# Kernel tuning notes

Hardware: AMD Instinct MI355X
Metric: run time of the kernel (lower is better)

## Reference

```python
import jax, jax.numpy as jnp
import numpy as np

N_NODES = 50000
N_EDGES = 800000
HID = 64
OUT = 64
REL = 5


def setup_inputs() -> dict:
    key = jax.random.key(0)
    ks = jax.random.split(key, 9)
    s_in = 1.0 / np.sqrt(HID)
    return {
        "contagion_risk": jax.random.normal(ks[0], (N_NODES, HID), jnp.float32),
        "edge_weight": jax.random.uniform(ks[1], (N_EDGES,), jnp.float32),
        # torch Linear weights stored transposed as [in, out] so y = x @ W + b
        "W_in_w": jax.random.uniform(ks[2], (HID, HID), jnp.float32, -s_in, s_in),
        "W_in_b": jax.random.uniform(ks[3], (HID,), jnp.float32, -s_in, s_in),
        "W_rel": jax.random.uniform(ks[4], (REL, HID, HID), jnp.float32, -s_in, s_in),
        "W_out_w": jax.random.uniform(ks[5], (HID, OUT), jnp.float32, -s_in, s_in),
        "W_out_b": jax.random.uniform(ks[6], (OUT,), jnp.float32, -s_in, s_in),
        "edge_index": jax.random.randint(ks[7], (2, N_EDGES), 0, N_NODES, jnp.int64 if jax.config.jax_enable_x64 else jnp.int32),
        "edge_type": jax.random.randint(ks[8], (N_EDGES,), 0, REL, jnp.int32),
        "num_nodes": N_NODES,
    }


def _dan_forward(contagion_risk, W_in_w, W_in_b, W_rel, W_out_w, W_out_b,
                 edge_index, edge_type, num_nodes):
    row, col = edge_index[0], edge_index[1]  # dst, src
    x = contagion_risk @ W_in_w + W_in_b                       # [N, H]
    x_j = x[col]                                               # [E, H] gather

    # gcn_norm (no self loops, unit edge weights): deg over col
    ones = jnp.ones(col.shape[0], x.dtype)
    deg = jax.ops.segment_sum(ones, col, num_segments=num_nodes)
    dis = jnp.where(deg > 0, jax.lax.rsqrt(jnp.maximum(deg, 1.0)), 0.0)
    norm_w = (dis[row] * dis[col])[:, None]                    # [E, 1]
    msg_gcn = jax.ops.segment_sum(x_j * norm_w, row, num_segments=num_nodes)

    # per-relation masked GEMM (grouped GEMM over REL relation types)
    res = jnp.zeros_like(x_j)
    for i in range(W_rel.shape[0]):
        mask = (edge_type == i)[:, None]
        res = res + jnp.where(mask, x_j @ W_rel[i], 0.0)

    # segment softmax over destination-node groups (per feature channel)
    seg_max = jax.ops.segment_max(res, row, num_segments=num_nodes)
    e = jnp.exp(res - seg_max[row])
    seg_sum = jax.ops.segment_sum(e, row, num_segments=num_nodes)
    weig = e / (seg_sum[row] + 1e-16)

    msg = jax.ops.segment_sum(res * weig, row, num_segments=num_nodes)
    out = (msg_gcn + 0.5 * jax.nn.relu(msg)) @ W_out_w + W_out_b
    return out


def reference(contagion_risk, edge_weight, W_in_w, W_in_b, W_rel, W_out_w, W_out_b,
              edge_index, edge_type, num_nodes):
    # edge_weight is accepted by the original forward but never used
    return _dan_forward(contagion_risk, W_in_w, W_in_b, W_rel, W_out_w, W_out_b,
                        edge_index, edge_type, num_nodes)
```

## Files before the change

### kernel.cpp

```cpp
#include <hip/hip_runtime.h>
#include <hip/hip_bf16.h>

#define HID 64
#define REL 5
#define EPB 2048

typedef short bf16x8 __attribute__((ext_vector_type(8)));
typedef float f32x4 __attribute__((ext_vector_type(4)));

__device__ __forceinline__ float bf2f(unsigned short u) {
    return __uint_as_float(((unsigned)u) << 16);
}
__device__ __forceinline__ unsigned short f2bf(float f) {
    __hip_bfloat16 h = (__hip_bfloat16)f;
    return *(unsigned short*)&h;
}
__device__ __forceinline__ void dec_edge(const int* __restrict__ ei, int i64,
                                         int E, int e, int& r, int& c) {
    if (i64) { r = ei[2 * e]; c = ei[2 * (E + e)]; }
    else     { r = ei[e];     c = ei[E + e]; }
}

__global__ void k_detect(const unsigned short* __restrict__ wb,
                         const int* __restrict__ ei, int* flags) {
    int lane = threadIdx.x;
    bool big = (lane < 32) ? (fabsf(bf2f(wb[2 * lane])) > 0.26f) : false;
    unsigned long long b1 = __ballot(big);
    bool odd_nz = (ei[2 * lane + 1] != 0);
    unsigned long long b2 = __ballot(odd_nz);
    if (lane == 0) {
        flags[0] = (b1 != 0ull) ? 1 : 0;
        flags[1] = (b2 == 0ull) ? 1 : 0;
    }
}

__global__ void k_pack(const void* Win, const void* bin, const void* Wr,
                       const void* Wout, const void* bout,
                       unsigned short* __restrict__ Bpk,
                       float* __restrict__ binf, float* __restrict__ boutf,
                       const int* __restrict__ flags) {
    int f = flags[0];
    int gid = blockIdx.x * 256 + threadIdx.x;
    if (gid < 7 * 2 * 4 * 64) {
        int lane = gid & 63;
        int nt = (gid >> 6) & 3;
        int ks = (gid >> 8) & 1;
        int mat = gid >> 9;
        int q = lane >> 4, n = nt * 16 + (lane & 15);
#pragma unroll
        for (int j = 0; j < 8; j++) {
            int k = ks * 32 + q * 8 + j;
            int idx = k * 64 + n;
            float val;
            if (mat == 0)
                val = f ? ((const float*)Win)[idx] : bf2f(((const unsigned short*)Win)[idx]);
            else if (mat <= 5) {
                int ii = (mat - 1) * 4096 + idx;
                val = f ? ((const float*)Wr)[ii] : bf2f(((const unsigned short*)Wr)[ii]);
            } else
                val = f ? ((const float*)Wout)[idx] : bf2f(((const unsigned short*)Wout)[idx]);
            Bpk[(size_t)gid * 8 + j] = f2bf(val);
        }
    }
    if (gid < 64)
        binf[gid] = f ? ((const float*)bin)[gid] : bf2f(((const unsigned short*)bin)[gid]);
    else if (gid >= 64 && gid < 128) {
        int i = gid - 64;
        boutf[i] = f ? ((const float*)bout)[i] : bf2f(((const unsigned short*)bout)[i]);
    }
}

__global__ void k_p1a(const int* __restrict__ ei, const int* __restrict__ flags,
                      int* __restrict__ hist, int E, int NB, int nblk) {
    extern __shared__ int lh[];
    int tid = threadIdx.x, blk = blockIdx.x;
    for (int i = tid; i < 2 * NB; i += 256) lh[i] = 0;
    __syncthreads();
    int i64 = flags[1];
#pragma unroll
    for (int k = 0; k < EPB / 256; k++) {
        int e = blk * EPB + k * 256 + tid;
        if (e < E) {
            int r, c;
            dec_edge(ei, i64, E, e, r, c);
            atomicAdd(&lh[r >> 6], 1);
            atomicAdd(&lh[NB + (c >> 6)], 1);
        }
    }
    __syncthreads();
    size_t NBn = (size_t)NB * nblk;
    for (int i = tid; i < NB; i += 256) {
        hist[(size_t)i * nblk + blk] = lh[i];
        hist[NBn + (size_t)i * nblk + blk] = lh[NB + i];
    }
}

__global__ void s_blk(const int* __restrict__ v, int* __restrict__ bsum, int M) {
    __shared__ int red[256];
    int t = threadIdx.x;
    int i0 = blockIdx.x * 1024 + t * 4;
    int s = 0;
#pragma unroll
    for (int j = 0; j < 4; j++) { int i = i0 + j; if (i < M) s += v[i]; }
    red[t] = s;
    __syncthreads();
    for (int d = 128; d > 0; d >>= 1) {
        if (t < d) red[t] += red[t + d];
        __syncthreads();
    }
    if (t == 0) bsum[blockIdx.x] = red[0];
}

__global__ void s_top(int* __restrict__ bsum, int nsb) {
    __shared__ int v[1024];
    int t = threadIdx.x;
    for (int i = t; i < nsb; i += 256) v[i] = bsum[i];
    __syncthreads();
    if (t == 0) {
        int run = 0;
        for (int i = 0; i < nsb; i++) { int x = v[i]; v[i] = run; run += x; }
    }
    __syncthreads();
    for (int i = t; i < nsb; i += 256) bsum[i] = v[i];
}

__global__ void s_apply(int* __restrict__ v, const int* __restrict__ bsum, int M) {
    __shared__ int red[256];
    int t = threadIdx.x;
    int i0 = blockIdx.x * 1024 + t * 4;
    int x[4];
    int s = 0;
#pragma unroll
    for (int j = 0; j < 4; j++) {
        int i = i0 + j;
        x[j] = (i < M) ? v[i] : 0;
        s += x[j];
    }
    red[t] = s;
    __syncthreads();
    for (int d = 1; d < 256; d <<= 1) {
        int add = (t >= d) ? red[t - d] : 0;
        __syncthreads();
        red[t] += add;
        __syncthreads();
    }
    int run = bsum[blockIdx.x] + red[t] - s;
#pragma unroll
    for (int j = 0; j < 4; j++) {
        int i = i0 + j;
        if (i < M) { int tmp = x[j]; v[i] = run; run += tmp; }
    }
}

__global__ void k_p1c(const int* __restrict__ ei, const int* __restrict__ et,
                      const int* __restrict__ flags, const int* __restrict__ hist,
                      unsigned* __restrict__ rbuf, unsigned char* __restrict__ cb8,
                      int E, int NB, int nblk) {
    extern __shared__ int lh[];
    int tid = threadIdx.x, blk = blockIdx.x;
    for (int i = tid; i < 2 * NB; i += 256) lh[i] = 0;
    __syncthreads();
    int i64 = flags[1];
    size_t NBn = (size_t)NB * nblk;
#pragma unroll
    for (int k = 0; k < EPB / 256; k++) {
        int e = blk * EPB + k * 256 + tid;
        if (e < E) {
            int r, c;
            dec_edge(ei, i64, E, e, r, c);
            int t = et[e];
            int binR = r >> 6;
            int posR = hist[(size_t)binR * nblk + blk] + atomicAdd(&lh[binR], 1);
            rbuf[posR] = ((unsigned)(r & 63) << 26) | ((unsigned)t << 17) | (unsigned)c;
            int binC = c >> 6;
            int posC = hist[NBn + (size_t)binC * nblk + blk] - E + atomicAdd(&lh[NB + binC], 1);
            cb8[posC] = (unsigned char)(c & 63);
        }
    }
}

__global__ void k_p2r(const unsigned* __restrict__ rbuf, const int* __restrict__ hist,
                      int* __restrict__ off, unsigned* __restrict__ edata4,
                      int E, int N, int NB, int nblk) {
    __shared__ int lcnt[64], excl[64], lcnt2[64];
    int tid = threadIdx.x, bk = blockIdx.x;
    int bstart = hist[(size_t)bk * nblk];
    int bend = (bk + 1 < NB) ? hist[(size_t)(bk + 1) * nblk] : E;
    if (tid < 64) { lcnt[tid] = 0; lcnt2[tid] = 0; }
    __syncthreads();
    for (int e = bstart + tid; e < bend; e += 256)
        atomicAdd(&lcnt[rbuf[e] >> 26], 1);
    __syncthreads();
    if (tid == 0) {
        int run = 0;
        for (int j = 0; j < 64; j++) { excl[j] = run; run += lcnt[j]; }
    }
    __syncthreads();
    if (tid < 64) {
        int node = bk * 64 + tid;
        if (node < N) off[node] = bstart + excl[tid];
    }
    if (bk == 0 && tid == 0) off[N] = E;
    for (int e = bstart + tid; e < bend; e += 256) {
        unsigned rec = rbuf[e];
        int rl = rec >> 26;
        int t = (rec >> 17) & 7;
        int c = rec & 0x1FFFF;
        int pos = bstart + excl[rl] + atomicAdd(&lcnt2[rl], 1);
        edata4[pos] = (unsigned)c | ((unsigned)t << 20);
    }
}

__global__ void k_p2c(const unsigned char* __restrict__ cb8, const int* __restrict__ hist,
                      float* __restrict__ dis, int E, int NB, int nblk) {
    __shared__ int lcnt[64];
    int tid = threadIdx.x, bk = blockIdx.x;
    size_t NBn = (size_t)NB * nblk;
    int cstart = hist[NBn + (size_t)bk * nblk] - E;
    int cend = (bk + 1 < NB) ? hist[NBn + (size_t)(bk + 1) * nblk] - E : E;
    if (tid < 64) lcnt[tid] = 0;
    __syncthreads();
    for (int e = cstart + tid; e < cend; e += 256)
        atomicAdd(&lcnt[cb8[e]], 1);
    __syncthreads();
    if (tid < 64) {
        int node = bk * 64 + tid;
        int d = lcnt[tid];
        dis[node] = (d > 0) ? rsqrtf((float)d) : 0.f;
    }
}

__device__ __forceinline__ bf16x8 load_a8(const void* A, int f, size_t base) {
    if (f) {
        const float* Af = (const float*)A + base;
        bf16x8 r;
#pragma unroll
        for (int j = 0; j < 8; j++) r[j] = (short)f2bf(Af[j]);
        return r;
    }
    return *(const bf16x8*)((const unsigned short*)A + base);
}

__global__ void __launch_bounds__(256)
k_xy(const void* __restrict__ A, const unsigned short* __restrict__ Bpk,
     const float* __restrict__ binf, const float* __restrict__ dis,
     unsigned short* __restrict__ Yb, const int* __restrict__ flags,
     int N, int Np) {
    __shared__ unsigned short Bs[6 * 2 * 4 * 64 * 8];
    __shared__ unsigned short Xs[64 * 64];
    __shared__ unsigned short Ys[64 * 64];
    __shared__ float bs[64];
    int tid = threadIdx.x;
    for (int i = tid; i < 6 * 2 * 4 * 64; i += 256)
        ((uint4*)Bs)[i] = ((const uint4*)Bpk)[i];
    if (tid < 64) bs[tid] = binf[tid];
    __syncthreads();

    int w = tid >> 6, lane = tid & 63;
    int q = lane >> 4, n16 = lane & 15;
    int mrow = w * 16 + n16;
    int f = flags[0];
    int arow = min(blockIdx.x * 64 + mrow, N - 1);
    bf16x8 a0 = load_a8(A, f, (size_t)arow * 64 + 8 * q);
    bf16x8 a1 = load_a8(A, f, (size_t)arow * 64 + 8 * q + 32);

    float disv[4];
#pragma unroll
    for (int r = 0; r < 4; r++) {
        int node = blockIdx.x * 64 + w * 16 + 4 * q + r;
        disv[r] = dis[node];
    }

    size_t snode = (size_t)(blockIdx.x * 64 + mrow);

#pragma unroll
    for (int nt = 0; nt < 4; nt++) {
        f32x4 d = {0.f, 0.f, 0.f, 0.f};
        bf16x8 b0 = *(const bf16x8*)(Bs + (size_t)(((0 * 2 + 0) * 4 + nt) * 64 + lane) * 8);
        bf16x8 b1 = *(const bf16x8*)(Bs + (size_t)(((0 * 2 + 1) * 4 + nt) * 64 + lane) * 8);
        d = __builtin_amdgcn_mfma_f32_16x16x32_bf16(a0, b0, d, 0, 0, 0);
        d = __builtin_amdgcn_mfma_f32_16x16x32_bf16(a1, b1, d, 0, 0, 0);
        int col = nt * 16 + n16;
#pragma unroll
        for (int r = 0; r < 4; r++) {
            int rowl = w * 16 + 4 * q + r;
            float xval = d[r] + bs[col];
            Xs[rowl * 64 + col] = f2bf(xval);
            Ys[rowl * 64 + col] = f2bf(xval * disv[r]);
        }
    }
    {
        unsigned short* dst = Yb + ((size_t)5 * Np + snode) * 64;
        *(bf16x8*)(dst + 8 * q)      = *(const bf16x8*)(Ys + mrow * 64 + 8 * q);
        *(bf16x8*)(dst + 8 * q + 32) = *(const bf16x8*)(Ys + mrow * 64 + 8 * q + 32);
    }
    bf16x8 a20 = *(const bf16x8*)(Xs + mrow * 64 + 8 * q);
    bf16x8 a21 = *(const bf16x8*)(Xs + mrow * 64 + 8 * q + 32);

    for (int rel = 0; rel < REL; rel++) {
        int mat = 1 + rel;
#pragma unroll
        for (int nt = 0; nt < 4; nt++) {
            f32x4 d = {0.f, 0.f, 0.f, 0.f};
            bf16x8 b0 = *(const bf16x8*)(Bs + (size_t)(((mat * 2 + 0) * 4 + nt) * 64 + lane) * 8);
            bf16x8 b1 = *(const bf16x8*)(Bs + (size_t)(((mat * 2 + 1) * 4 + nt) * 64 + lane) * 8);
            d = __builtin_amdgcn_mfma_f32_16x16x32_bf16(a20, b0, d, 0, 0, 0);
            d = __builtin_amdgcn_mfma_f32_16x16x32_bf16(a21, b1, d, 0, 0, 0);
            int col = nt * 16 + n16;
#pragma unroll
            for (int r = 0; r < 4; r++)
                Ys[(w * 16 + 4 * q + r) * 64 + col] = f2bf(d[r]);
        }
        unsigned short* dst = Yb + ((size_t)rel * Np + snode) * 64;
        *(bf16x8*)(dst + 8 * q)      = *(const bf16x8*)(Ys + mrow * 64 + 8 * q);
        *(bf16x8*)(dst + 8 * q + 32) = *(const bf16x8*)(Ys + mrow * 64 + 8 * q + 32);
    }
}

__global__ void __launch_bounds__(256)
k_main(const unsigned short* __restrict__ Yb, const int* __restrict__ off,
       const unsigned* __restrict__ edata4, const float* __restrict__ dis,
       unsigned short* __restrict__ v, int N, int Np) {
    int tid = threadIdx.x;
    int wv = tid >> 6, lane = tid & 63;
    int n = blockIdx.x * 4 + wv;
    if (n >= N) return;
    int half = lane >> 5;
    int c2 = (lane & 31) * 2;
    int e0 = off[n], e1 = off[n + 1];
    float s0 = 0.f, s1 = 0.f, u0 = 0.f, u1 = 0.f, g0 = 0.f, g1 = 0.f;
    float s0b = 0.f, s1b = 0.f, u0b = 0.f, u1b = 0.f, g0b = 0.f, g1b = 0.f;
    const unsigned short* Yx = Yb + (size_t)5 * Np * 64;

    int e = e0 + half;
    for (; e + 2 < e1; e += 4) {
        unsigned mda = edata4[e];
        unsigned mdb = edata4[e + 2];
        int ca = mda & 0xFFFFF, ta = mda >> 20;
        int cb = mdb & 0xFFFFF, tb = mdb >> 20;
        unsigned yva = *(const unsigned*)(Yb + ((size_t)ta * Np + ca) * 64 + c2);
        unsigned xva = *(const unsigned*)(Yx + (size_t)ca * 64 + c2);
        unsigned yvb = *(const unsigned*)(Yb + ((size_t)tb * Np + cb) * 64 + c2);
        unsigned xvb = *(const unsigned*)(Yx + (size_t)cb * 64 + c2);
        float r0 = __uint_as_float(yva << 16);
        float r1 = __uint_as_float(yva & 0xFFFF0000u);
        g0 += __uint_as_float(xva << 16);
        g1 += __uint_as_float(xva & 0xFFFF0000u);
        float p0 = __expf(fminf(r0, 60.f));
        float p1 = __expf(fminf(r1, 60.f));
        s0 += p0; s1 += p1;
        u0 += r0 * p0; u1 += r1 * p1;
        float r0b = __uint_as_float(yvb << 16);
        float r1b = __uint_as_float(yvb & 0xFFFF0000u);
        g0b += __uint_as_float(xvb << 16);
        g1b += __uint_as_float(xvb & 0xFFFF0000u);
        float p0b = __expf(fminf(r0b, 60.f));
        float p1b = __expf(fminf(r1b, 60.f));
        s0b += p0b; s1b += p1b;
        u0b += r0b * p0b; u1b += r1b * p1b;
    }
    if (e < e1) {
        unsigned md = edata4[e];
        int c = md & 0xFFFFF, t = md >> 20;
        unsigned yv = *(const unsigned*)(Yb + ((size_t)t * Np + c) * 64 + c2);
        unsigned xv = *(const unsigned*)(Yx + (size_t)c * 64 + c2);
        float r0 = __uint_as_float(yv << 16);
        float r1 = __uint_as_float(yv & 0xFFFF0000u);
        g0 += __uint_as_float(xv << 16);
        g1 += __uint_as_float(xv & 0xFFFF0000u);
        float p0 = __expf(fminf(r0, 60.f));
        float p1 = __expf(fminf(r1, 60.f));
        s0 += p0; s1 += p1;
        u0 += r0 * p0; u1 += r1 * p1;
    }
    s0 += s0b; s1 += s1b; u0 += u0b; u1 += u1b; g0 += g0b; g1 += g1b;

    s0 += __shfl_xor(s0, 32); s1 += __shfl_xor(s1, 32);
    u0 += __shfl_xor(u0, 32); u1 += __shfl_xor(u1, 32);
    g0 += __shfl_xor(g0, 32); g1 += __shfl_xor(g1, 32);
    if (half == 0) {
        float dn = dis[n];
        float m0 = u0 / (s0 + 1e-16f), m1 = u1 / (s1 + 1e-16f);
        float v0 = g0 * dn + 0.5f * fmaxf(m0, 0.f);
        float v1 = g1 * dn + 0.5f * fmaxf(m1, 0.f);
        unsigned pack = (unsigned)f2bf(v0) | ((unsigned)f2bf(v1) << 16);
        *(unsigned*)(v + (size_t)n * 64 + c2) = pack;
    }
}

__global__ void __launch_bounds__(256)
k_out(const unsigned short* __restrict__ v, const unsigned short* __restrict__ Bpk,
      const float* __restrict__ boutf, void* __restrict__ outv,
      const int* __restrict__ flags, int N, int Np) {
    __shared__ unsigned short Bs[2 * 4 * 64 * 8];
    __shared__ float Os[64 * 64];
    __shared__ float bs[64];
    int tid = threadIdx.x;
    const unsigned short* src = Bpk + (size_t)6 * 2 * 4 * 64 * 8;
    for (int i = tid; i < 2 * 4 * 64; i += 256)
        ((uint4*)Bs)[i] = ((const uint4*)src)[i];
    if (tid < 64) bs[tid] = boutf[tid];
    __syncthreads();

    int w = tid >> 6, lane = tid & 63;
    int q = lane >> 4, n16 = lane & 15;
    int mrow = w * 16 + n16;
    int arow = min(blockIdx.x * 64 + mrow, N - 1);
    bf16x8 a0 = *(const bf16x8*)(v + (size_t)arow * 64 + 8 * q);
    bf16x8 a1 = *(const bf16x8*)(v + (size_t)arow * 64 + 8 * q + 32);
    int f = flags[0];
#pragma unroll
    for (int nt = 0; nt < 4; nt++) {
        f32x4 d = {0.f, 0.f, 0.f, 0.f};
        bf16x8 b0 = *(const bf16x8*)(Bs + (size_t)((0 * 4 + nt) * 64 + lane) * 8);
        bf16x8 b1 = *(const bf16x8*)(Bs + (size_t)((1 * 4 + nt) * 64 + lane) * 8);
        d = __builtin_amdgcn_mfma_f32_16x16x32_bf16(a0, b0, d, 0, 0, 0);
        d = __builtin_amdgcn_mfma_f32_16x16x32_bf16(a1, b1, d, 0, 0, 0);
        int col = nt * 16 + n16;
#pragma unroll
        for (int r = 0; r < 4; r++)
            Os[(w * 16 + 4 * q + r) * 64 + col] = d[r] + bs[col];
    }
    int node = blockIdx.x * 64 + mrow;
    if (node < N) {
        if (f) {
            float* dst = (float*)outv + (size_t)node * 64;
#pragma unroll
            for (int cchunk = 0; cchunk < 2; cchunk++) {
                int c0 = 8 * q + 32 * cchunk;
                *(f32x4*)(dst + c0)     = *(const f32x4*)(Os + mrow * 64 + c0);
                *(f32x4*)(dst + c0 + 4) = *(const f32x4*)(Os + mrow * 64 + c0 + 4);
            }
        } else {
            unsigned short* dst = (unsigned short*)outv + (size_t)node * 64;
#pragma unroll
            for (int cchunk = 0; cchunk < 2; cchunk++) {
                int c0 = 8 * q + 32 * cchunk;
                bf16x8 pk;
#pragma unroll
                for (int j = 0; j < 8; j++)
                    pk[j] = (short)f2bf(Os[mrow * 64 + c0 + j]);
                *(bf16x8*)(dst + c0) = pk;
            }
        }
    }
}

extern "C" void kernel_launch(void* const* d_in, const int* in_sizes, int n_in,
                              void* d_out, int out_size, void* d_ws, size_t ws_size,
                              hipStream_t stream) {
    const void* A    = d_in[0];
    const void* Win  = d_in[2];
    const void* bin  = d_in[3];
    const void* Wrel = d_in[4];
    const void* Wout = d_in[5];
    const void* bout = d_in[6];
    const int* ei = (const int*)d_in[7];
    const int* et = (const int*)d_in[8];
    int N = in_sizes[0] / HID;
    int E = in_sizes[8];
    int Np = ((N + 63) / 64) * 64;
    int NB = Np / 64;
    int nblk = (E + EPB - 1) / EPB;
    int M = 2 * NB * nblk;
    int nsb = (M + 1023) / 1024;

    char* p = (char*)d_ws;
    auto carve = [&](size_t bytes) {
        char* q = p;
        p += (bytes + 15) & ~(size_t)15;
        return q;
    };
    unsigned short* Yb   = (unsigned short*)carve((size_t)6 * Np * 64 * 2);
    unsigned short* vv   = (unsigned short*)carve((size_t)Np * 64 * 2);
    unsigned*       rbuf = (unsigned*)carve((size_t)E * 4);
    unsigned char*  cb8  = (unsigned char*)carve((size_t)E);
    unsigned*       edata4 = (unsigned*)carve((size_t)E * 4);
    int*            hist = (int*)carve((size_t)M * 4);
    unsigned short* Bpk  = (unsigned short*)carve((size_t)7 * 4096 * 2);
    float* binf  = (float*)carve(64 * 4);
    float* boutf = (float*)carve(64 * 4);
    int* off     = (int*)carve((size_t)(N + 1) * 4);
    float* dis   = (float*)carve((size_t)Np * 4);
    int* bsum    = (int*)carve((size_t)nsb * 4);
    int* flags   = (int*)carve(16);

    size_t lds_part = (size_t)2 * NB * 4;

    k_detect<<<1, 64, 0, stream>>>((const unsigned short*)bin, ei, flags);
    k_pack<<<14, 256, 0, stream>>>(Win, bin, Wrel, Wout, bout, Bpk, binf, boutf, flags);
    k_p1a<<<nblk, 256, lds_part, stream>>>(ei, flags, hist, E, NB, nblk);
    s_blk<<<nsb, 256, 0, stream>>>(hist, bsum, M);
    s_top<<<1, 256, 0, stream>>>(bsum, nsb);
    s_apply<<<nsb, 256, 0, stream>>>(hist, bsum, M);
    k_p1c<<<nblk, 256, lds_part, stream>>>(ei, et, flags, hist, rbuf, cb8, E, NB, nblk);
    k_p2r<<<NB, 256, 0, stream>>>(rbuf, hist, off, edata4, E, N, NB, nblk);
    k_p2c<<<NB, 256, 0, stream>>>(cb8, hist, dis, E, NB, nblk);
    k_xy<<<Np / 64, 256, 0, stream>>>(A, Bpk, binf, dis, Yb, flags, N, Np);
    k_main<<<(N + 3) / 4, 256, 0, stream>>>(Yb, off, edata4, dis, vv, N, Np);
    k_out<<<Np / 64, 256, 0, stream>>>(vv, Bpk, boutf, d_out, flags, N, Np);
}
```

Measured before the change: 215.4 us.

## Interleave scaled-x into per-relation Y rows, widen sort buckets, merge p2 kernels

k_xy now writes each relation's output interleaved with the dis-scaled x row into a 128-wide buffer. k_main can then fetch the relation value and the GCN term for an edge in one 8-byte gather instead of two separate 4-byte gathers from different arrays, which cuts random memory transactions. The counting sort now uses 256-node buckets and 4096 edges per block, and the row and column second-pass kernels are merged into one launch. The cost is writing x five times (once per relation), so the Y buffer footprint grows while the separate x slab is dropped.

```diff
diff --git a/kernel.cpp b/kernel.cpp
--- a/kernel.cpp
+++ b/kernel.cpp
@@ -3,7 +3,8 @@
 
 #define HID 64
 #define REL 5
-#define EPB 2048
+#define EPB 4096
+#define BKT 256
 
 typedef short bf16x8 __attribute__((ext_vector_type(8)));
 typedef float f32x4 __attribute__((ext_vector_type(4)));
@@ -83,15 +84,15 @@
         if (e < E) {
             int r, c;
             dec_edge(ei, i64, E, e, r, c);
-            atomicAdd(&lh[r >> 6], 1);
-            atomicAdd(&lh[NB + (c >> 6)], 1);
-        }
-    }
-    __syncthreads();
-    size_t NBn = (size_t)NB * nblk;
+            atomicAdd(&lh[r >> 8], 1);
+            atomicAdd(&lh[NB + (c >> 8)], 1);
+        }
+    }
+    __syncthreads();
+    int NBn = NB * nblk;
     for (int i = tid; i < NB; i += 256) {
-        hist[(size_t)i * nblk + blk] = lh[i];
-        hist[NBn + (size_t)i * nblk + blk] = lh[NB + i];
+        hist[i * nblk + blk] = lh[i];
+        hist[NBn + i * nblk + blk] = lh[NB + i];
     }
 }
 
@@ -161,7 +162,7 @@
     for (int i = tid; i < 2 * NB; i += 256) lh[i] = 0;
     __syncthreads();
     int i64 = flags[1];
-    size_t NBn = (size_t)NB * nblk;
+    int NBn = NB * nblk;
 #pragma unroll
     for (int k = 0; k < EPB / 256; k++) {
         int e = blk * EPB + k * 256 + tid;
@@ -169,62 +170,65 @@
             int r, c;
             dec_edge(ei, i64, E, e, r, c);
             int t = et[e];
-            int binR = r >> 6;
-            int posR = hist[(size_t)binR * nblk + blk] + atomicAdd(&lh[binR], 1);
-            rbuf[posR] = ((unsigned)(r & 63) << 26) | ((unsigned)t << 17) | (unsigned)c;
-            int binC = c >> 6;
-            int posC = hist[NBn + (size_t)binC * nblk + blk] - E + atomicAdd(&lh[NB + binC], 1);
-            cb8[posC] = (unsigned char)(c & 63);
-        }
-    }
-}
-
-__global__ void k_p2r(const unsigned* __restrict__ rbuf, const int* __restrict__ hist,
-                      int* __restrict__ off, unsigned* __restrict__ edata4,
-                      int E, int N, int NB, int nblk) {
-    __shared__ int lcnt[64], excl[64], lcnt2[64];
-    int tid = threadIdx.x, bk = blockIdx.x;
-    int bstart = hist[(size_t)bk * nblk];
-    int bend = (bk + 1 < NB) ? hist[(size_t)(bk + 1) * nblk] : E;
-    if (tid < 64) { lcnt[tid] = 0; lcnt2[tid] = 0; }
-    __syncthreads();
-    for (int e = bstart + tid; e < bend; e += 256)
-        atomicAdd(&lcnt[rbuf[e] >> 26], 1);
-    __syncthreads();
-    if (tid == 0) {
-        int run = 0;
-        for (int j = 0; j < 64; j++) { excl[j] = run; run += lcnt[j]; }
-    }
-    __syncthreads();
-    if (tid < 64) {
-        int node = bk * 64 + tid;
-        if (node < N) off[node] = bstart + excl[tid];
-    }
-    if (bk == 0 && tid == 0) off[N] = E;
-    for (int e = bstart + tid; e < bend; e += 256) {
-        unsigned rec = rbuf[e];
-        int rl = rec >> 26;
-        int t = (rec >> 17) & 7;
-        int c = rec & 0x1FFFF;
-        int pos = bstart + excl[rl] + atomicAdd(&lcnt2[rl], 1);
-        edata4[pos] = (unsigned)c | ((unsigned)t << 20);
-    }
-}
-
-__global__ void k_p2c(const unsigned char* __restrict__ cb8, const int* __restrict__ hist,
-                      float* __restrict__ dis, int E, int NB, int nblk) {
-    __shared__ int lcnt[64];
-    int tid = threadIdx.x, bk = blockIdx.x;
-    size_t NBn = (size_t)NB * nblk;
-    int cstart = hist[NBn + (size_t)bk * nblk] - E;
-    int cend = (bk + 1 < NB) ? hist[NBn + (size_t)(bk + 1) * nblk] - E : E;
-    if (tid < 64) lcnt[tid] = 0;
-    __syncthreads();
-    for (int e = cstart + tid; e < cend; e += 256)
-        atomicAdd(&lcnt[cb8[e]], 1);
-    __syncthreads();
-    if (tid < 64) {
-        int node = bk * 64 + tid;
+            int binR = r >> 8;
+            int posR = hist[binR * nblk + blk] + atomicAdd(&lh[binR], 1);
+            rbuf[posR] = ((unsigned)(r & 255) << 20) | ((unsigned)t << 17) | (unsigned)c;
+            int binC = c >> 8;
+            int posC = hist[NBn + binC * nblk + blk] - E + atomicAdd(&lh[NB + binC], 1);
+            cb8[posC] = (unsigned char)(c & 255);
+        }
+    }
+}
+
+__global__ void k_p2(const unsigned* __restrict__ rbuf, const unsigned char* __restrict__ cb8,
+                     const int* __restrict__ hist,
+                     int* __restrict__ off, unsigned* __restrict__ edata4,
+                     float* __restrict__ dis, int E, int N, int NB, int nblk) {
+    __shared__ int lcnt[BKT], excl[BKT], lcnt2[BKT];
+    int tid = threadIdx.x;
+    int bk = blockIdx.x;
+    if (bk < NB) {
+        int bstart = hist[bk * nblk];
+        int bend = (bk + 1 < NB) ? hist[(bk + 1) * nblk] : E;
+        lcnt[tid] = 0; lcnt2[tid] = 0;
+        __syncthreads();
+        for (int e = bstart + tid; e < bend; e += 256)
+            atomicAdd(&lcnt[(rbuf[e] >> 20) & 255], 1);
+        __syncthreads();
+        int s = lcnt[tid];
+        excl[tid] = s;
+        __syncthreads();
+        for (int d = 1; d < 256; d <<= 1) {
+            int add = (tid >= d) ? excl[tid - d] : 0;
+            __syncthreads();
+            excl[tid] += add;
+            __syncthreads();
+        }
+        int base = excl[tid] - s;
+        excl[tid] = base;
+        __syncthreads();
+        int node = bk * BKT + tid;
+        if (node < N) off[node] = bstart + base;
+        if (bk == 0 && tid == 0) off[N] = E;
+        for (int e = bstart + tid; e < bend; e += 256) {
+            unsigned rec = rbuf[e];
+            int rl = (rec >> 20) & 255;
+            int t = (rec >> 17) & 7;
+            int c = rec & 0x1FFFF;
+            int pos = bstart + excl[rl] + atomicAdd(&lcnt2[rl], 1);
+            edata4[pos] = (unsigned)c | ((unsigned)t << 20);
+        }
+    } else {
+        int bk2 = bk - NB;
+        int NBn = NB * nblk;
+        int cstart = hist[NBn + bk2 * nblk] - E;
+        int cend = (bk2 + 1 < NB) ? hist[NBn + (bk2 + 1) * nblk] - E : E;
+        lcnt[tid] = 0;
+        __syncthreads();
+        for (int e = cstart + tid; e < cend; e += 256)
+            atomicAdd(&lcnt[cb8[e]], 1);
+        __syncthreads();
+        int node = bk2 * BKT + tid;
         int d = lcnt[tid];
         dis[node] = (d > 0) ? rsqrtf((float)d) : 0.f;
     }
@@ -244,10 +248,11 @@
 __global__ void __launch_bounds__(256)
 k_xy(const void* __restrict__ A, const unsigned short* __restrict__ Bpk,
      const float* __restrict__ binf, const float* __restrict__ dis,
-     unsigned short* __restrict__ Yb, const int* __restrict__ flags,
+     unsigned short* __restrict__ Yi, const int* __restrict__ flags,
      int N, int Np) {
     __shared__ unsigned short Bs[6 * 2 * 4 * 64 * 8];
     __shared__ unsigned short Xs[64 * 64];
+    __shared__ unsigned short Xss[64 * 64];
     __shared__ unsigned short Ys[64 * 64];
     __shared__ float bs[64];
     int tid = threadIdx.x;
@@ -286,13 +291,8 @@
             int rowl = w * 16 + 4 * q + r;
             float xval = d[r] + bs[col];
             Xs[rowl * 64 + col] = f2bf(xval);
-            Ys[rowl * 64 + col] = f2bf(xval * disv[r]);
-        }
-    }
-    {
-        unsigned short* dst = Yb + ((size_t)5 * Np + snode) * 64;
-        *(bf16x8*)(dst + 8 * q)      = *(const bf16x8*)(Ys + mrow * 64 + 8 * q);
-        *(bf16x8*)(dst + 8 * q + 32) = *(const bf16x8*)(Ys + mrow * 64 + 8 * q + 32);
+            Xss[rowl * 64 + col] = f2bf(xval * disv[r]);
+        }
     }
     bf16x8 a20 = *(const bf16x8*)(Xs + mrow * 64 + 8 * q);
     bf16x8 a21 = *(const bf16x8*)(Xs + mrow * 64 + 8 * q + 32);
@@ -311,14 +311,26 @@
             for (int r = 0; r < 4; r++)
                 Ys[(w * 16 + 4 * q + r) * 64 + col] = f2bf(d[r]);
         }
-        unsigned short* dst = Yb + ((size_t)rel * Np + snode) * 64;
-        *(bf16x8*)(dst + 8 * q)      = *(const bf16x8*)(Ys + mrow * 64 + 8 * q);
-        *(bf16x8*)(dst + 8 * q + 32) = *(const bf16x8*)(Ys + mrow * 64 + 8 * q + 32);
+        unsigned short* dst = Yi + ((size_t)rel * Np + snode) * 128;
+#pragma unroll
+        for (int ch = 0; ch < 2; ch++) {
+            int c0 = 8 * q + 32 * ch;
+            bf16x8 y8 = *(const bf16x8*)(Ys + mrow * 64 + c0);
+            bf16x8 x8 = *(const bf16x8*)(Xss + mrow * 64 + c0);
+            bf16x8 lo, hi;
+#pragma unroll
+            for (int j = 0; j < 4; j++) {
+                lo[2 * j] = y8[j];     lo[2 * j + 1] = x8[j];
+                hi[2 * j] = y8[4 + j]; hi[2 * j + 1] = x8[4 + j];
+            }
+            *(bf16x8*)(dst + 2 * c0)     = lo;
+            *(bf16x8*)(dst + 2 * c0 + 8) = hi;
+        }
     }
 }
 
 __global__ void __launch_bounds__(256)
-k_main(const unsigned short* __restrict__ Yb, const int* __restrict__ off,
+k_main(const unsigned short* __restrict__ Yi, const int* __restrict__ off,
        const unsigned* __restrict__ edata4, const float* __restrict__ dis,
        unsigned short* __restrict__ v, int N, int Np) {
     int tid = threadIdx.x;
@@ -326,11 +338,10 @@
     int n = blockIdx.x * 4 + wv;
     if (n >= N) return;
     int half = lane >> 5;
-    int c2 = (lane & 31) * 2;
+    int co = (lane & 31) * 4;
     int e0 = off[n], e1 = off[n + 1];
     float s0 = 0.f, s1 = 0.f, u0 = 0.f, u1 = 0.f, g0 = 0.f, g1 = 0.f;
     float s0b = 0.f, s1b = 0.f, u0b = 0.f, u1b = 0.f, g0b = 0.f, g1b = 0.f;
-    const unsigned short* Yx = Yb + (size_t)5 * Np * 64;
 
     int e = e0 + half;
     for (; e + 2 < e1; e += 4) {
@@ -338,22 +349,20 @@
         unsigned mdb = edata4[e + 2];
         int ca = mda & 0xFFFFF, ta = mda >> 20;
         int cb = mdb & 0xFFFFF, tb = mdb >> 20;
-        unsigned yva = *(const unsigned*)(Yb + ((size_t)ta * Np + ca) * 64 + c2);
-        unsigned xva = *(const unsigned*)(Yx + (size_t)ca * 64 + c2);
-        unsigned yvb = *(const unsigned*)(Yb + ((size_t)tb * Np + cb) * 64 + c2);
-        unsigned xvb = *(const unsigned*)(Yx + (size_t)cb * 64 + c2);
-        float r0 = __uint_as_float(yva << 16);
-        float r1 = __uint_as_float(yva & 0xFFFF0000u);
-        g0 += __uint_as_float(xva << 16);
-        g1 += __uint_as_float(xva & 0xFFFF0000u);
+        uint2 ya = *(const uint2*)(Yi + ((size_t)ta * Np + ca) * 128 + co);
+        uint2 yb = *(const uint2*)(Yi + ((size_t)tb * Np + cb) * 128 + co);
+        float r0 = __uint_as_float(ya.x << 16);
+        float r1 = __uint_as_float(ya.y << 16);
+        g0 += __uint_as_float(ya.x & 0xFFFF0000u);
+        g1 += __uint_as_float(ya.y & 0xFFFF0000u);
         float p0 = __expf(fminf(r0, 60.f));
         float p1 = __expf(fminf(r1, 60.f));
         s0 += p0; s1 += p1;
         u0 += r0 * p0; u1 += r1 * p1;
-        float r0b = __uint_as_float(yvb << 16);
-        float r1b = __uint_as_float(yvb & 0xFFFF0000u);
-        g0b += __uint_as_float(xvb << 16);
-        g1b += __uint_as_float(xvb & 0xFFFF0000u);
+        float r0b = __uint_as_float(yb.x << 16);
+        float r1b = __uint_as_float(yb.y << 16);
+        g0b += __uint_as_float(yb.x & 0xFFFF0000u);
+        g1b += __uint_as_float(yb.y & 0xFFFF0000u);
         float p0b = __expf(fminf(r0b, 60.f));
         float p1b = __expf(fminf(r1b, 60.f));
         s0b += p0b; s1b += p1b;
@@ -362,12 +371,11 @@
     if (e < e1) {
         unsigned md = edata4[e];
         int c = md & 0xFFFFF, t = md >> 20;
-        unsigned yv = *(const unsigned*)(Yb + ((size_t)t * Np + c) * 64 + c2);
-        unsigned xv = *(const unsigned*)(Yx + (size_t)c * 64 + c2);
-        float r0 = __uint_as_float(yv << 16);
-        float r1 = __uint_as_float(yv & 0xFFFF0000u);
-        g0 += __uint_as_float(xv << 16);
-        g1 += __uint_as_float(xv & 0xFFFF0000u);
+        uint2 ya = *(const uint2*)(Yi + ((size_t)t * Np + c) * 128 + co);
+        float r0 = __uint_as_float(ya.x << 16);
+        float r1 = __uint_as_float(ya.y << 16);
+        g0 += __uint_as_float(ya.x & 0xFFFF0000u);
+        g1 += __uint_as_float(ya.y & 0xFFFF0000u);
         float p0 = __expf(fminf(r0, 60.f));
         float p1 = __expf(fminf(r1, 60.f));
         s0 += p0; s1 += p1;
@@ -384,7 +392,7 @@
         float v0 = g0 * dn + 0.5f * fmaxf(m0, 0.f);
         float v1 = g1 * dn + 0.5f * fmaxf(m1, 0.f);
         unsigned pack = (unsigned)f2bf(v0) | ((unsigned)f2bf(v1) << 16);
-        *(unsigned*)(v + (size_t)n * 64 + c2) = pack;
+        *(unsigned*)(v + (size_t)n * 64 + (lane & 31) * 2) = pack;
     }
 }
 
@@ -459,8 +467,8 @@
     const int* et = (const int*)d_in[8];
     int N = in_sizes[0] / HID;
     int E = in_sizes[8];
-    int Np = ((N + 63) / 64) * 64;
-    int NB = Np / 64;
+    int Np = ((N + BKT - 1) / BKT) * BKT;
+    int NB = Np / BKT;
     int nblk = (E + EPB - 1) / EPB;
     int M = 2 * NB * nblk;
     int nsb = (M + 1023) / 1024;
@@ -471,7 +479,7 @@
         p += (bytes + 15) & ~(size_t)15;
         return q;
     };
-    unsigned short* Yb   = (unsigned short*)carve((size_t)6 * Np * 64 * 2);
+    unsigned short* Yi   = (unsigned short*)carve((size_t)REL * Np * 128 * 2);
     unsigned short* vv   = (unsigned short*)carve((size_t)Np * 64 * 2);
     unsigned*       rbuf = (unsigned*)carve((size_t)E * 4);
     unsigned char*  cb8  = (unsigned char*)carve((size_t)E);
@@ -494,9 +502,8 @@
     s_top<<<1, 256, 0, stream>>>(bsum, nsb);
     s_apply<<<nsb, 256, 0, stream>>>(hist, bsum, M);
     k_p1c<<<nblk, 256, lds_part, stream>>>(ei, et, flags, hist, rbuf, cb8, E, NB, nblk);
-    k_p2r<<<NB, 256, 0, stream>>>(rbuf, hist, off, edata4, E, N, NB, nblk);
-    k_p2c<<<NB, 256, 0, stream>>>(cb8, hist, dis, E, NB, nblk);
-    k_xy<<<Np / 64, 256, 0, stream>>>(A, Bpk, binf, dis, Yb, flags, N, Np);
-    k_main<<<(N + 3) / 4, 256, 0, stream>>>(Yb, off, edata4, dis, vv, N, Np);
+    k_p2<<<2 * NB, 256, 0, stream>>>(rbuf, cb8, hist, off, edata4, dis, E, N, NB, nblk);
+    k_xy<<<Np / 64, 256, 0, stream>>>(A, Bpk, binf, dis, Yi, flags, N, Np);
+    k_main<<<(N + 3) / 4, 256, 0, stream>>>(Yi, off, edata4, dis, vv, N, Np);
     k_out<<<Np / 64, 256, 0, stream>>>(vv, Bpk, boutf, d_out, flags, N, Np);
 }
```

Measured after the change: 201.2 us. -6.6%, faster.
